# Optimization experiments

Measured on AMD Instinct MI355X. Metric: run time of the kernel, lower is better.

The kernel has to match this reference:

```python
import jax, jax.numpy as jnp
import numpy as np

MARGIN = 0.4
ALPHA = 0.01


def _pairwise_dist(emb):
    sq = jnp.sum(emb * emb, axis=1)
    d2 = jnp.maximum(sq[:, None] + sq[None, :] - 2.0 * (emb @ emb.T), 0.0)
    safe = jnp.where(d2 > 0, d2, 1.0)
    return jnp.where(d2 > 0, jnp.sqrt(safe), 0.0)


def setup_inputs() -> dict:
    key = jax.random.key(0)
    ka, kp, kn = jax.random.split(key, 3)
    B, D = 4096, 128
    return {
        "a": jax.random.normal(ka, (B, D), dtype=jnp.float32),
        "p": jax.random.normal(kp, (B, D), dtype=jnp.float32),
        "n": jax.random.normal(kn, (B, D), dtype=jnp.float32),
    }


def reference(a, p, n):
    B = a.shape[0]
    emb = jnp.concatenate([a, p, n], axis=0)            # [3B, D]
    labels = jnp.tile(jnp.arange(B), 3)                 # [3B]
    dist = _pairwise_dist(emb)                          # [3B, 3B]
    same = labels[:, None] == labels[None, :]           # exactly 3 True per row (incl. diag)
    # Every row has >=2 positives (3 incl. self) and >=1 negative, so all rows count.
    pos_max = jnp.max(jnp.where(same, dist, -jnp.inf), axis=1)
    neg_min = jnp.min(jnp.where(same, jnp.inf, dist), axis=1)
    loss = jnp.mean(jnp.maximum(pos_max - neg_min + MARGIN, 0.0))
    reg = jnp.mean((jnp.abs(emb) - 1.0) ** 2)
    return loss + ALPHA * reg
```

## Files before the change

### kernel.cpp

```cpp
#include <hip/hip_runtime.h>

#define NROWS 12288
#define BSZ   4096
#define DIM   128
#define CSPLIT 16
#define COLS_PER_BLOCK (NROWS / CSPLIT)
#define NSTRIPS (COLS_PER_BLOCK / 32)

typedef __bf16 bf16x8 __attribute__((ext_vector_type(8)));
typedef float  f32x4  __attribute__((ext_vector_type(4)));

__device__ __forceinline__ unsigned short f2bf(float f) {
  unsigned int u = __float_as_uint(f);
  u = u + 0x7FFFu + ((u >> 16) & 1u);
  return (unsigned short)(u >> 16);
}
__device__ __forceinline__ float bf2f(unsigned short h) {
  return __uint_as_float(((unsigned int)h) << 16);
}

__global__ void prep_k(const float* __restrict__ a, const float* __restrict__ p,
                       const float* __restrict__ nn,
                       unsigned short* __restrict__ embh, float* __restrict__ sq,
                       unsigned int* __restrict__ negbits,
                       float* __restrict__ posmax2, float* __restrict__ regpart) {
  const int w = threadIdx.x >> 6, lane = threadIdx.x & 63;
  const int i = blockIdx.x * 4 + w;
  const float2 av = reinterpret_cast<const float2*>(a  + (size_t)i * DIM)[lane];
  const float2 pv = reinterpret_cast<const float2*>(p  + (size_t)i * DIM)[lane];
  const float2 nv = reinterpret_cast<const float2*>(nn + (size_t)i * DIM)[lane];

  const unsigned short ha0 = f2bf(av.x), ha1 = f2bf(av.y);
  const unsigned short hp0 = f2bf(pv.x), hp1 = f2bf(pv.y);
  const unsigned short hn0 = f2bf(nv.x), hn1 = f2bf(nv.y);
  reinterpret_cast<ushort2*>(embh + (size_t)i * DIM)[lane]             = make_ushort2(ha0, ha1);
  reinterpret_cast<ushort2*>(embh + (size_t)(BSZ + i) * DIM)[lane]     = make_ushort2(hp0, hp1);
  reinterpret_cast<ushort2*>(embh + (size_t)(2 * BSZ + i) * DIM)[lane] = make_ushort2(hn0, hn1);

  float rax = bf2f(ha0), ray = bf2f(ha1);
  float rpx = bf2f(hp0), rpy = bf2f(hp1);
  float rnx = bf2f(hn0), rny = bf2f(hn1);
  float sa = rax * rax + ray * ray;
  float sp = rpx * rpx + rpy * rpy;
  float sn = rnx * rnx + rny * rny;

  float t0 = fabsf(av.x) - 1.f, t1 = fabsf(av.y) - 1.f;
  float t2 = fabsf(pv.x) - 1.f, t3 = fabsf(pv.y) - 1.f;
  float t4 = fabsf(nv.x) - 1.f, t5 = fabsf(nv.y) - 1.f;
  float rg = t0 * t0 + t1 * t1 + t2 * t2 + t3 * t3 + t4 * t4 + t5 * t5;

  float dx, dy;
  dx = av.x - pv.x; dy = av.y - pv.y; float dap = dx * dx + dy * dy;
  dx = av.x - nv.x; dy = av.y - nv.y; float dan = dx * dx + dy * dy;
  dx = pv.x - nv.x; dy = pv.y - nv.y; float dpn = dx * dx + dy * dy;

  for (int m = 32; m; m >>= 1) {
    sa  += __shfl_xor(sa, m);  sp  += __shfl_xor(sp, m);  sn  += __shfl_xor(sn, m);
    rg  += __shfl_xor(rg, m);
    dap += __shfl_xor(dap, m); dan += __shfl_xor(dan, m); dpn += __shfl_xor(dpn, m);
  }
  if (lane == 0) {
    sq[i] = sa; sq[BSZ + i] = sp; sq[2 * BSZ + i] = sn;
    negbits[i] = negbits[BSZ + i] = negbits[2 * BSZ + i] = 0x7F800000u;
    posmax2[i]           = fmaxf(dap, dan);
    posmax2[BSZ + i]     = fmaxf(dap, dpn);
    posmax2[2 * BSZ + i] = fmaxf(dan, dpn);
    regpart[i] = rg;
  }
}

__global__ __launch_bounds__(256, 3) void negmin_k(
    const unsigned short* __restrict__ embh,
    const float* __restrict__ sq,
    unsigned int* __restrict__ negbits) {
  __shared__ __align__(16) char ldsB[2][8192];
  const int tid  = threadIdx.x;
  const int w    = tid >> 6;
  const int lane = tid & 63;
  const int c16  = lane & 15;
  const int q    = lane >> 4;
  const int wRow    = blockIdx.x * 256 + w * 64;
  const int colBase = blockIdx.y * COLS_PER_BLOCK;
  const int rot     = blockIdx.x % NSTRIPS;

  bf16x8 afrag[4][4];
  {
    const char* abase = (const char*)embh + (size_t)(wRow + c16) * 256 + q * 16;
#pragma unroll
    for (int mt = 0; mt < 4; ++mt)
#pragma unroll
      for (int ks = 0; ks < 4; ++ks)
        afrag[mt][ks] = *reinterpret_cast<const bf16x8*>(abase + mt * 4096 + ks * 64);
  }

  float minv[4][4];
#pragma unroll
  for (int mt = 0; mt < 4; ++mt)
#pragma unroll
    for (int r = 0; r < 4; ++r) minv[mt][r] = __builtin_inff();

  auto stage = [&](int sidx, int b) {
#pragma unroll
    for (int h = 0; h < 2; ++h) {
      const int kc = w * 2 + h;
      const char* gp = (const char*)embh +
          (size_t)(colBase + sidx * 32 + (kc & 1) * 16 + c16) * 256 +
          (kc >> 1) * 64 + q * 16;
      __builtin_amdgcn_global_load_lds(
          (const __attribute__((address_space(1))) unsigned int*)gp,
          (__attribute__((address_space(3))) unsigned int*)(&ldsB[b][kc * 1024]),
          16, 0, 0);
    }
  };

  int strip = rot;
  stage(strip, 0);
  __syncthreads();
  {
    int s1 = strip + 1; if (s1 >= NSTRIPS) s1 -= NSTRIPS;
    stage(s1, 1);
  }

  for (int c = 0; c < NSTRIPS; ++c) {
    const int b = c & 1;
    const int colStart = colBase + strip * 32;
    const float sq0 = sq[colStart + c16];
    const float sq1 = sq[colStart + 16 + c16];

    f32x4 acc[4][2] = {};
#pragma unroll
    for (int ks = 0; ks < 4; ++ks)
#pragma unroll
      for (int ct = 0; ct < 2; ++ct) {
        const bf16x8 bfr =
            *reinterpret_cast<const bf16x8*>(&ldsB[b][(ks * 2 + ct) * 1024 + lane * 16]);
#pragma unroll
        for (int mt = 0; mt < 4; ++mt)
          acc[mt][ct] =
              __builtin_amdgcn_mfma_f32_16x16x32_bf16(afrag[mt][ks], bfr, acc[mt][ct], 0, 0, 0);
      }

    __syncthreads();
    if (c + 2 < NSTRIPS) {
      int s2 = strip + 2; if (s2 >= NSTRIPS) s2 -= NSTRIPS;
      stage(s2, b);
    }

    const int dd = (colStart - wRow) & 4095;
    if (dd < 76 || dd > 4064) {
#pragma unroll
      for (int mt = 0; mt < 4; ++mt)
#pragma unroll
        for (int ct = 0; ct < 2; ++ct) {
          const float sqb = ct ? sq1 : sq0;
          const int lvc = dd + ct * 16 + c16 - q * 4;
#pragma unroll
          for (int r = 0; r < 4; ++r) {
            float v = fmaf(-2.f, acc[mt][ct][r], sqb);
            const int K = mt * 16 + r;
            if (lvc == K || lvc == K + 4096) v = __builtin_inff();
            minv[mt][r] = fminf(minv[mt][r], v);
          }
        }
    } else {
#pragma unroll
      for (int mt = 0; mt < 4; ++mt)
#pragma unroll
        for (int ct = 0; ct < 2; ++ct) {
          const float sqb = ct ? sq1 : sq0;
#pragma unroll
          for (int r = 0; r < 4; ++r)
            minv[mt][r] = fminf(minv[mt][r], fmaf(-2.f, acc[mt][ct][r], sqb));
        }
    }

    strip = strip + 1; if (strip >= NSTRIPS) strip -= NSTRIPS;
  }

#pragma unroll
  for (int mt = 0; mt < 4; ++mt)
#pragma unroll
    for (int r = 0; r < 4; ++r) {
      float v = minv[mt][r];
      v = fminf(v, __shfl_xor(v, 1));
      v = fminf(v, __shfl_xor(v, 2));
      v = fminf(v, __shfl_xor(v, 4));
      v = fminf(v, __shfl_xor(v, 8));
      if (c16 == 0) {
        const int row = wRow + mt * 16 + q * 4 + r;
        float d2 = sq[row] + v;
        d2 = fmaxf(d2, 0.f);
        atomicMin(&negbits[row], __float_as_uint(d2));
      }
    }
}

__global__ void final_k(const float* __restrict__ posmax2,
                        const unsigned int* __restrict__ negbits,
                        const float* __restrict__ regpart, float* __restrict__ out) {
  __shared__ float red[16], redr[16];
  const int tid = threadIdx.x;
  float s = 0.f;
  for (int i = tid; i < NROWS; i += 1024) {
    const float pm = sqrtf(posmax2[i]);
    const float nm = sqrtf(__uint_as_float(negbits[i]));
    s += fmaxf(pm - nm + 0.4f, 0.f);
  }
  float rg = 0.f;
  for (int i = tid; i < BSZ; i += 1024) rg += regpart[i];
  for (int m = 32; m; m >>= 1) { s += __shfl_xor(s, m); rg += __shfl_xor(rg, m); }
  if ((tid & 63) == 0) { red[tid >> 6] = s; redr[tid >> 6] = rg; }
  __syncthreads();
  if (tid == 0) {
    float t = 0.f, tr = 0.f;
#pragma unroll
    for (int k = 0; k < 16; ++k) { t += red[k]; tr += redr[k]; }
    out[0] = t / (float)NROWS + 0.01f * (tr / (float)(NROWS * DIM));
  }
}

extern "C" void kernel_launch(void* const* d_in, const int* in_sizes, int n_in,
                              void* d_out, int out_size, void* d_ws, size_t ws_size,
                              hipStream_t stream) {
  const float* a  = (const float*)d_in[0];
  const float* p  = (const float*)d_in[1];
  const float* nn = (const float*)d_in[2];
  float* out = (float*)d_out;
  char* ws = (char*)d_ws;

  const size_t EMBH_BYTES = (size_t)NROWS * DIM * 2;
  unsigned short* embh    = (unsigned short*)ws;
  float*          sq      = (float*)(ws + EMBH_BYTES);
  unsigned int*   negbit  = (unsigned int*)(ws + EMBH_BYTES + (size_t)NROWS * 4);
  float*          pos2    = (float*)(ws + EMBH_BYTES + (size_t)NROWS * 8);
  float*          regpart = (float*)(ws + EMBH_BYTES + (size_t)NROWS * 12);

  prep_k<<<BSZ / 4, 256, 0, stream>>>(a, p, nn, embh, sq, negbit, pos2, regpart);
  negmin_k<<<dim3(NROWS / 256, CSPLIT), 256, 0, stream>>>(embh, sq, negbit);
  final_k<<<1, 1024, 0, stream>>>(pos2, negbit, regpart, out);
}
```

Baseline: 112.9 us.

## Exploit distance-matrix symmetry by computing only upper-triangular tiles

Replaces the full row-by-column-split grid with a launch over the upper-triangular 256x256 tiles of the symmetric distance matrix. Each off-diagonal tile updates the row minima and also reduces column minima through shared memory, writing both with atomicMin. Row squared norms are now added per element so column minima are complete. This roughly halves the MFMA work, at the cost of extra per-element min operations, shuffles, LDS traffic and more atomics.

```diff
diff --git a/kernel.cpp b/kernel.cpp
--- a/kernel.cpp
+++ b/kernel.cpp
@@ -3,8 +3,9 @@
 #define NROWS 12288
 #define BSZ   4096
 #define DIM   128
-#define CSPLIT 16
-#define COLS_PER_BLOCK (NROWS / CSPLIT)
+#define NB    48
+#define NTILES (NB * (NB + 1) / 2)
+#define COLS_PER_BLOCK 256
 #define NSTRIPS (COLS_PER_BLOCK / 32)
 
 typedef __bf16 bf16x8 __attribute__((ext_vector_type(8)));
@@ -74,14 +75,20 @@
     const float* __restrict__ sq,
     unsigned int* __restrict__ negbits) {
   __shared__ __align__(16) char ldsB[2][8192];
+  __shared__ float cminw[4][COLS_PER_BLOCK];
   const int tid  = threadIdx.x;
   const int w    = tid >> 6;
   const int lane = tid & 63;
   const int c16  = lane & 15;
   const int q    = lane >> 4;
-  const int wRow    = blockIdx.x * 256 + w * 64;
-  const int colBase = blockIdx.y * COLS_PER_BLOCK;
-  const int rot     = blockIdx.x % NSTRIPS;
+
+  int rem = blockIdx.x, ti = 0;
+  while (rem >= NB - ti) { rem -= NB - ti; ++ti; }
+  const int tj   = ti + rem;
+  const bool diag = (ti == tj);
+  const int wRow    = ti * 256 + w * 64;
+  const int colBase = tj * 256;
+  const int rot     = blockIdx.x & (NSTRIPS - 1);
 
   bf16x8 afrag[4][4];
   {
@@ -91,6 +98,17 @@
 #pragma unroll
       for (int ks = 0; ks < 4; ++ks)
         afrag[mt][ks] = *reinterpret_cast<const bf16x8*>(abase + mt * 4096 + ks * 64);
+  }
+
+  float sqrow[4][4];
+  {
+    const int rbase = wRow + q * 4;
+#pragma unroll
+    for (int mt = 0; mt < 4; ++mt) {
+      const f32x4 t = *reinterpret_cast<const f32x4*>(&sq[rbase + mt * 16]);
+#pragma unroll
+      for (int r = 0; r < 4; ++r) sqrow[mt][r] = t[r];
+    }
   }
 
   float minv[4][4];
@@ -147,6 +165,7 @@
     }
 
     const int dd = (colStart - wRow) & 4095;
+    float cf0 = __builtin_inff(), cf1 = __builtin_inff();
     if (dd < 76 || dd > 4064) {
 #pragma unroll
       for (int mt = 0; mt < 4; ++mt)
@@ -156,10 +175,11 @@
           const int lvc = dd + ct * 16 + c16 - q * 4;
 #pragma unroll
           for (int r = 0; r < 4; ++r) {
-            float v = fmaf(-2.f, acc[mt][ct][r], sqb);
+            float e = fmaf(-2.f, acc[mt][ct][r], sqb) + sqrow[mt][r];
             const int K = mt * 16 + r;
-            if (lvc == K || lvc == K + 4096) v = __builtin_inff();
-            minv[mt][r] = fminf(minv[mt][r], v);
+            if (lvc == K || lvc == K + 4096) e = __builtin_inff();
+            minv[mt][r] = fminf(minv[mt][r], e);
+            if (ct) cf1 = fminf(cf1, e); else cf0 = fminf(cf0, e);
           }
         }
     } else {
@@ -169,9 +189,23 @@
         for (int ct = 0; ct < 2; ++ct) {
           const float sqb = ct ? sq1 : sq0;
 #pragma unroll
-          for (int r = 0; r < 4; ++r)
-            minv[mt][r] = fminf(minv[mt][r], fmaf(-2.f, acc[mt][ct][r], sqb));
+          for (int r = 0; r < 4; ++r) {
+            float e = fmaf(-2.f, acc[mt][ct][r], sqb) + sqrow[mt][r];
+            minv[mt][r] = fminf(minv[mt][r], e);
+            if (ct) cf1 = fminf(cf1, e); else cf0 = fminf(cf0, e);
+          }
         }
+    }
+
+    if (!diag) {
+      cf0 = fminf(cf0, __shfl_xor(cf0, 16));
+      cf0 = fminf(cf0, __shfl_xor(cf0, 32));
+      cf1 = fminf(cf1, __shfl_xor(cf1, 16));
+      cf1 = fminf(cf1, __shfl_xor(cf1, 32));
+      if (q == 0) {
+        cminw[w][strip * 32 + c16]      = cf0;
+        cminw[w][strip * 32 + 16 + c16] = cf1;
+      }
     }
 
     strip = strip + 1; if (strip >= NSTRIPS) strip -= NSTRIPS;
@@ -188,11 +222,16 @@
       v = fminf(v, __shfl_xor(v, 8));
       if (c16 == 0) {
         const int row = wRow + mt * 16 + q * 4 + r;
-        float d2 = sq[row] + v;
-        d2 = fmaxf(d2, 0.f);
-        atomicMin(&negbits[row], __float_as_uint(d2));
+        atomicMin(&negbits[row], __float_as_uint(fmaxf(v, 0.f)));
       }
     }
+
+  __syncthreads();
+  if (!diag) {
+    const float m = fminf(fminf(cminw[0][tid], cminw[1][tid]),
+                          fminf(cminw[2][tid], cminw[3][tid]));
+    atomicMin(&negbits[colBase + tid], __float_as_uint(fmaxf(m, 0.f)));
+  }
 }
 
 __global__ void final_k(const float* __restrict__ posmax2,
@@ -236,6 +275,6 @@
   float*          regpart = (float*)(ws + EMBH_BYTES + (size_t)NROWS * 12);
 
   prep_k<<<BSZ / 4, 256, 0, stream>>>(a, p, nn, embh, sq, negbit, pos2, regpart);
-  negmin_k<<<dim3(NROWS / 256, CSPLIT), 256, 0, stream>>>(embh, sq, negbit);
+  negmin_k<<<dim3(NTILES), 256, 0, stream>>>(embh, sq, negbit);
   final_k<<<1, 1024, 0, stream>>>(pos2, negbit, regpart, out);
 }
```

Result: faster. 108.7 us (-3.7%).
